# Kernel tuning notes

Measured on AMD Instinct MI355X. Metric: run time of the kernel, lower is better.

Reference implementation:

```python
import jax, jax.numpy as jnp
import numpy as np

N_HEADS = 16

def setup_inputs() -> dict:
    key = jax.random.key(0)
    ks = jax.random.split(key, 5)
    C = 1024
    B, T = 2, 2048
    s_in = 1.0 / np.sqrt(C)
    x = jax.random.normal(ks[0], (B, T, C), dtype=jnp.float32)
    W_qkv = jax.random.normal(ks[1], (C, 3 * C), dtype=jnp.float32) * s_in
    b_qkv = jnp.zeros((3 * C,), dtype=jnp.float32)
    W_proj = jax.random.normal(ks[2], (C, C), dtype=jnp.float32) * s_in
    b_proj = jnp.zeros((C,), dtype=jnp.float32)
    return {"x": x, "W_qkv": W_qkv, "b_qkv": b_qkv, "W_proj": W_proj, "b_proj": b_proj}

def reference(x, W_qkv, b_qkv, W_proj, b_proj):
    B, T, C = x.shape
    H = N_HEADS
    D = C // H  # head dim
    qkv = x @ W_qkv + b_qkv                      # [B,T,3C]
    q, k, v = jnp.split(qkv, 3, axis=-1)
    # [B,T,C] -> [B,H,T,D]
    q = q.reshape(B, T, H, D).transpose(0, 2, 1, 3)
    k = k.reshape(B, T, H, D).transpose(0, 2, 1, 3)
    v = v.reshape(B, T, H, D).transpose(0, 2, 1, 3)
    scale = 1.0 / np.sqrt(D)
    att = jnp.einsum('bhqd,bhkd->bhqk', q, k) * scale  # [B,H,T,T]
    causal = jnp.tril(jnp.ones((T, T), dtype=bool))
    att = jnp.where(causal[None, None], att, -jnp.inf)
    att = jax.nn.softmax(att, axis=-1)
    y = jnp.einsum('bhqk,bhkd->bhqd', att, v)    # [B,H,T,D]
    y = y.transpose(0, 2, 1, 3).reshape(B, T, C)
    return y @ W_proj + b_proj
```

## Files before the change

kernel.cpp:

```cpp
#include <hip/hip_runtime.h>
#include <hip/hip_bf16.h>
#include <stdint.h>

#define DEVI __device__ __forceinline__

typedef __attribute__((ext_vector_type(8))) short bf16x8;
typedef __attribute__((ext_vector_type(4))) float f32x4;
typedef __attribute__((ext_vector_type(4))) short short4v;
typedef __attribute__((ext_vector_type(4))) float float4v;
typedef __attribute__((ext_vector_type(2))) unsigned int uint2v;

#define QSCALE 0.1803368801111204f

DEVI unsigned short f2bf(float f) {
  union { float f; unsigned u; } v; v.f = f;
  unsigned r = v.u + 0x7FFFu + ((v.u >> 16) & 1u);
  return (unsigned short)(r >> 16);
}

DEVI unsigned cvt_pk_bf16(float lo, float hi) {
  unsigned r;
  asm("v_cvt_pk_bf16_f32 %0, %1, %2" : "=v"(r) : "v"(lo), "v"(hi));
  return r;
}

DEVI void async16(unsigned short* lds, const unsigned short* g) {
  __builtin_amdgcn_global_load_lds(
      (const __attribute__((address_space(1))) void*)g,
      (__attribute__((address_space(3))) void*)lds, 16, 0, 0);
}

DEVI int xcd_swz_flat() {
  int orig = (int)blockIdx.x + (int)gridDim.x * (int)blockIdx.y;
  int cpx = ((int)gridDim.x * (int)gridDim.y) >> 3;
  return (orig & 7) * cpx + (orig >> 3);
}

__global__ void k_f32_to_bf16(const float* __restrict__ in,
                              unsigned short* __restrict__ out, int n4) {
  int i = blockIdx.x * 256 + threadIdx.x;
  if (i < n4) {
    float4v f = *reinterpret_cast<const float4v*>(in + (size_t)i * 4);
    short4v o;
#pragma unroll
    for (int j = 0; j < 4; ++j) o[j] = (short)f2bf(f[j]);
    *reinterpret_cast<short4v*>(out + (size_t)i * 4) = o;
  }
}

__global__ void k_wt2(const float* __restrict__ Wq, const float* __restrict__ Wp,
                      unsigned short* __restrict__ WqT, unsigned short* __restrict__ WpT) {
  __shared__ float tile[32][33];
  const int bx = (int)blockIdx.x;
  const float* W;
  unsigned short* Wt;
  int N, n0;
  if (bx < 96) { W = Wq; Wt = WqT; N = 3072; n0 = bx * 32; }
  else         { W = Wp; Wt = WpT; N = 1024; n0 = (bx - 96) * 32; }
  const int K = 1024, k0 = (int)blockIdx.y * 32;
  int r = threadIdx.x >> 5, c = threadIdx.x & 31;
#pragma unroll
  for (int i = 0; i < 4; ++i)
    tile[r + i * 8][c] = W[(size_t)(k0 + r + i * 8) * N + n0 + c];
  __syncthreads();
#pragma unroll
  for (int i = 0; i < 4; ++i)
    Wt[(size_t)(n0 + r + i * 8) * K + k0 + c] = f2bf(tile[c][r + i * 8]);
}

DEVI void stage_ab(unsigned short* AsB, unsigned short* BsB,
                   const unsigned short* Ab, const unsigned short* Bb,
                   int K, int k0, int tid) {
#pragma unroll
  for (int it = 0; it < 2; ++it) {
    int c = it * 256 + tid;
    int row = c >> 2, cc = (c & 3) * 8;
    async16(&AsB[c * 8], Ab + (size_t)row * K + k0 + cc);
    async16(&BsB[c * 8], Bb + (size_t)row * K + k0 + cc);
  }
}

__global__ void k_gemm(const unsigned short* __restrict__ A,
                       const unsigned short* __restrict__ Bt,
                       const float* __restrict__ bias,
                       unsigned short* __restrict__ qkv,
                       unsigned short* __restrict__ vt,
                       int M, int N, int K) {
  __shared__ __align__(16) unsigned short As[2][128 * 32];
  __shared__ __align__(16) unsigned short Bs[2][128 * 32];
  const int tid = threadIdx.x;
  const int swzf = xcd_swz_flat();
  const int m0 = (swzf / (int)gridDim.x) * 128, n0 = (swzf % (int)gridDim.x) * 128;
  const int lane = tid & 63, w = tid >> 6;
  const int wr = (w >> 1) * 64, wc = (w & 1) * 64;
  const int lr = lane & 15, lg = lane >> 4;
  f32x4 acc[4][4] = {};
  const unsigned short* Ab = A + (size_t)m0 * K;
  const unsigned short* Bb = Bt + (size_t)n0 * K;

  const int ns = K >> 5;
  stage_ab(As[0], Bs[0], Ab, Bb, K, 0, tid);
  stage_ab(As[1], Bs[1], Ab, Bb, K, 32, tid);
  asm volatile("s_waitcnt vmcnt(4)" ::: "memory");
  __builtin_amdgcn_s_barrier();
  __builtin_amdgcn_sched_barrier(0);

  for (int s = 0; s < ns; ++s) {
    const int cur = s & 1;
    bf16x8 af[4], bfr[4];
#pragma unroll
    for (int m = 0; m < 4; ++m)
      af[m] = *reinterpret_cast<const bf16x8*>(&As[cur][(wr + m * 16 + lr) * 32 + lg * 8]);
#pragma unroll
    for (int n = 0; n < 4; ++n)
      bfr[n] = *reinterpret_cast<const bf16x8*>(&Bs[cur][(wc + n * 16 + lr) * 32 + lg * 8]);
#pragma unroll
    for (int m = 0; m < 4; ++m)
#pragma unroll
      for (int n = 0; n < 4; ++n)
        acc[m][n] = __builtin_amdgcn_mfma_f32_16x16x32_bf16(af[m], bfr[n], acc[m][n], 0, 0, 0);
    __builtin_amdgcn_s_barrier();
    const int ks = (s + 2 < ns) ? (s + 2) * 32 : 0;
    stage_ab(As[cur], Bs[cur], Ab, Bb, K, ks, tid);
    asm volatile("s_waitcnt vmcnt(4)" ::: "memory");
    __builtin_amdgcn_s_barrier();
    __builtin_amdgcn_sched_barrier(0);
  }
#pragma unroll
  for (int n = 0; n < 4; ++n) {
    int col = n0 + wc + n * 16 + lr;
    float bv = bias[col];
    int sel = col >> 10, cc = col & 1023;
    int h = cc >> 6, d = cc & 63;
    if (sel < 2) {
      float sc = (sel == 0) ? QSCALE : 1.0f;
#pragma unroll
      for (int m = 0; m < 4; ++m) {
#pragma unroll
        for (int r = 0; r < 4; ++r) {
          int row = m0 + wr + m * 16 + lg * 4 + r;
          int bh = ((row >> 11) << 4) + h;
          int t = row & 2047;
          qkv[((size_t)(sel * 32 + bh) * 2048 + t) * 64 + d] = f2bf((acc[m][n][r] + bv) * sc);
        }
      }
    } else {
#pragma unroll
      for (int m = 0; m < 4; ++m) {
        int row0 = m0 + wr + m * 16 + lg * 4;
        int bh = ((row0 >> 11) << 4) + h;
        int t0 = row0 & 2047;
        short4v pk;
#pragma unroll
        for (int r = 0; r < 4; ++r) pk[r] = (short)f2bf(acc[m][n][r] + bv);
        *reinterpret_cast<short4v*>(&vt[((size_t)(bh * 64 + d)) * 2048 + t0]) = pk;
      }
    }
  }
}

__global__ __launch_bounds__(256)
void k_gemmP(const unsigned short* __restrict__ A,
             const unsigned short* __restrict__ Bt,
             const float* __restrict__ bias,
             float* __restrict__ O, int M, int N, int K) {
  __shared__ __align__(16) unsigned short As[2][128 * 32];
  __shared__ __align__(16) unsigned short Bs[2][64 * 32];
  const int tid = threadIdx.x;
  const int swzf = xcd_swz_flat();
  const int m0 = (swzf / (int)gridDim.x) * 128, n0 = (swzf % (int)gridDim.x) * 64;
  const int lane = tid & 63, w = tid >> 6;
  const int wr = (w >> 1) * 64, wc = (w & 1) * 32;
  const int lr = lane & 15, lg = lane >> 4;
  f32x4 acc[4][2] = {};
  const unsigned short* Ab = A + (size_t)m0 * K;
  const unsigned short* Bb = Bt + (size_t)n0 * K;

  auto stage = [&](unsigned short* AsB, unsigned short* BsB, int k0) {
#pragma unroll
    for (int it = 0; it < 2; ++it) {
      int c = it * 256 + tid;
      int row = c >> 2, cc = (c & 3) * 8;
      async16(&AsB[c * 8], Ab + (size_t)row * K + k0 + cc);
    }
    int row = tid >> 2, cc = (tid & 3) * 8;
    async16(&BsB[tid * 8], Bb + (size_t)row * K + k0 + cc);
  };

  const int ns = K >> 5;
  stage(As[0], Bs[0], 0);
  stage(As[1], Bs[1], 32);
  asm volatile("s_waitcnt vmcnt(3)" ::: "memory");
  __builtin_amdgcn_s_barrier();
  __builtin_amdgcn_sched_barrier(0);

  for (int s = 0; s < ns; ++s) {
    const int cur = s & 1;
    bf16x8 af[4], bfr[2];
#pragma unroll
    for (int m = 0; m < 4; ++m)
      af[m] = *reinterpret_cast<const bf16x8*>(&As[cur][(wr + m * 16 + lr) * 32 + lg * 8]);
#pragma unroll
    for (int n = 0; n < 2; ++n)
      bfr[n] = *reinterpret_cast<const bf16x8*>(&Bs[cur][(wc + n * 16 + lr) * 32 + lg * 8]);
#pragma unroll
    for (int m = 0; m < 4; ++m)
#pragma unroll
      for (int n = 0; n < 2; ++n)
        acc[m][n] = __builtin_amdgcn_mfma_f32_16x16x32_bf16(af[m], bfr[n], acc[m][n], 0, 0, 0);
    __builtin_amdgcn_s_barrier();
    const int ks = (s + 2 < ns) ? (s + 2) * 32 : 0;
    stage(As[cur], Bs[cur], ks);
    asm volatile("s_waitcnt vmcnt(3)" ::: "memory");
    __builtin_amdgcn_s_barrier();
    __builtin_amdgcn_sched_barrier(0);
  }
#pragma unroll
  for (int n = 0; n < 2; ++n) {
    int col = n0 + wc + n * 16 + lr;
    float bv = bias[col];
#pragma unroll
    for (int m = 0; m < 4; ++m)
#pragma unroll
      for (int r = 0; r < 4; ++r) {
        int row = m0 + wr + m * 16 + lg * 4 + r;
        O[(size_t)row * N + col] = acc[m][n][r] + bv;
      }
  }
}

DEVI void stage_kv(unsigned short* KsB, unsigned short* VsB,
                   const unsigned short* Kbh, const unsigned short* Vbh,
                   int k0, int tid, int srow, int gcol) {
  async16(&KsB[tid * 8], Kbh + (size_t)(k0 + srow) * 64 + gcol);
  async16(&VsB[tid * 8], Vbh + (size_t)srow * 2048 + k0 + gcol);
}

DEVI void attn_store(unsigned short* __restrict__ Y, int bh, int qw, int lg, int lr,
                     const f32x4* o, float l_run) {
  const int b = bh >> 4, h = bh & 15;
  float rl = 1.0f / l_run;
  float rlo[4];
#pragma unroll
  for (int r = 0; r < 4; ++r) rlo[r] = __shfl(rl, lg * 4 + r, 64);
#pragma unroll
  for (int r = 0; r < 4; ++r) {
    int t = qw + lg * 4 + r;
#pragma unroll
    for (int n = 0; n < 4; ++n)
      Y[((size_t)(b * 2048 + t)) * 1024 + h * 64 + n * 16 + lr] = f2bf(o[n][r] * rlo[r]);
  }
}

__global__ __launch_bounds__(512)
void k_attn(const unsigned short* __restrict__ Qg,
            const unsigned short* __restrict__ Kg,
            const unsigned short* __restrict__ Vtg,
            unsigned short* __restrict__ Y) {
  __shared__ __align__(16) unsigned short Ks[2][64 * 64];
  __shared__ __align__(16) unsigned short Vs[2][64 * 64];
  __shared__ __align__(16) unsigned short Ps[8][16 * 64];
  const int orig = (int)blockIdx.x;
  const int slot = orig >> 8;
  const int within = orig & 255;
  const int sw = (within & 7) * 32 + (within >> 3);
  const int bh = sw >> 3;
  const int xp = sw & 7;
  const int x = slot ? xp : (15 - xp);
  const int nkt = 2 * x + 2;
  const int tid = threadIdx.x, lane = tid & 63, w = tid >> 6;
  const int lr = lane & 15, lg = lane >> 4;
  const int swz = (lane & 7) * 8;
  const int psw = (lr & 7) * 8;
  const unsigned short* Kbh = Kg + (size_t)bh * 2048 * 64;
  const unsigned short* Vbh = Vtg + (size_t)bh * 64 * 2048;

  const int qw = x * 128 + w * 16;
  const unsigned short* Qrow = Qg + ((size_t)bh * 2048 + qw + lr) * 64;
  bf16x8 qa0 = *reinterpret_cast<const bf16x8*>(&Qrow[lg * 8]);
  bf16x8 qa1 = *reinterpret_cast<const bf16x8*>(&Qrow[32 + lg * 8]);

  float m_run = -1e30f, l_run = 0.f;
  f32x4 o[4] = {};

  const int srow = tid >> 3;
  const int gcol = ((tid & 7) ^ (srow & 7)) * 8;

  stage_kv(Ks[0], Vs[0], Kbh, Vbh, 0, tid, srow, gcol);
  stage_kv(Ks[1], Vs[1], Kbh, Vbh, 64, tid, srow, gcol);
  asm volatile("s_waitcnt vmcnt(2)" ::: "memory");
  __builtin_amdgcn_s_barrier();
  __builtin_amdgcn_sched_barrier(0);

  for (int t = 0; t < nkt; ++t) {
    const int cur = t & 1;
    const int k0 = t * 64;
    if (k0 <= qw + 15) {
      const unsigned short* KsC = Ks[cur];
      const unsigned short* VsC = Vs[cur];

      f32x4 s[4];
      __builtin_amdgcn_s_setprio(1);
#pragma unroll
      for (int n = 0; n < 4; ++n) {
        bf16x8 kb0 = *reinterpret_cast<const bf16x8*>(&KsC[(n * 16 + lr) * 64 + ((lg * 8) ^ swz)]);
        bf16x8 kb1 = *reinterpret_cast<const bf16x8*>(&KsC[(n * 16 + lr) * 64 + ((32 + lg * 8) ^ swz)]);
        f32x4 z = {0.f, 0.f, 0.f, 0.f};
        z = __builtin_amdgcn_mfma_f32_16x16x32_bf16(kb0, qa0, z, 0, 0, 0);
        z = __builtin_amdgcn_mfma_f32_16x16x32_bf16(kb1, qa1, z, 0, 0, 0);
        s[n] = z;
      }
      __builtin_amdgcn_s_setprio(0);
      if (k0 + 63 > qw) {
        const int klim = qw + lr - k0 - lg * 4;
#pragma unroll
        for (int n = 0; n < 4; ++n)
#pragma unroll
          for (int r = 0; r < 4; ++r)
            if (n * 16 + r > klim) s[n][r] = -1e30f;
      }
      float tmax = s[0][0];
#pragma unroll
      for (int n = 0; n < 4; ++n)
#pragma unroll
        for (int r = 0; r < 4; ++r) tmax = fmaxf(tmax, s[n][r]);
      tmax = fmaxf(tmax, __shfl_xor(tmax, 16, 64));
      tmax = fmaxf(tmax, __shfl_xor(tmax, 32, 64));
      if (__any(tmax > m_run + 11.5f)) {
        float mNew = fmaxf(m_run, tmax);
        float alpha = __builtin_exp2f(m_run - mNew);
        m_run = mNew;
        l_run *= alpha;
        float ao[4];
#pragma unroll
        for (int r = 0; r < 4; ++r) ao[r] = __shfl(alpha, lg * 4 + r, 64);
#pragma unroll
        for (int n = 0; n < 4; ++n)
#pragma unroll
          for (int r = 0; r < 4; ++r) o[n][r] *= ao[r];
      }
      float tsum = 0.f;
#pragma unroll
      for (int n = 0; n < 4; ++n)
#pragma unroll
        for (int r = 0; r < 4; ++r) {
          s[n][r] = __builtin_exp2f(s[n][r] - m_run);
          tsum += s[n][r];
        }
      tsum += __shfl_xor(tsum, 16, 64);
      tsum += __shfl_xor(tsum, 32, 64);
      l_run += tsum;
#pragma unroll
      for (int n = 0; n < 4; ++n) {
        uint2v pk;
        pk[0] = cvt_pk_bf16(s[n][0], s[n][1]);
        pk[1] = cvt_pk_bf16(s[n][2], s[n][3]);
        *reinterpret_cast<uint2v*>(&Ps[w][lr * 64 + ((n * 16 + lg * 4) ^ psw)]) = pk;
      }
      __builtin_amdgcn_s_setprio(1);
#pragma unroll
      for (int jj = 0; jj < 2; ++jj) {
        bf16x8 pa = *reinterpret_cast<const bf16x8*>(&Ps[w][lr * 64 + ((jj * 32 + lg * 8) ^ psw)]);
#pragma unroll
        for (int n = 0; n < 4; ++n) {
          bf16x8 vb = *reinterpret_cast<const bf16x8*>(
              &VsC[(n * 16 + lr) * 64 + ((jj * 32 + lg * 8) ^ swz)]);
          o[n] = __builtin_amdgcn_mfma_f32_16x16x32_bf16(pa, vb, o[n], 0, 0, 0);
        }
      }
      __builtin_amdgcn_s_setprio(0);
    }
    __builtin_amdgcn_s_barrier();
    {
      const int ts = (t + 2 < nkt) ? (t + 2) : 0;
      stage_kv(Ks[cur], Vs[cur], Kbh, Vbh, ts * 64, tid, srow, gcol);
    }
    asm volatile("s_waitcnt vmcnt(2)" ::: "memory");
    __builtin_amdgcn_s_barrier();
    __builtin_amdgcn_sched_barrier(0);
  }
  attn_store(Y, bh, qw, lg, lr, o, l_run);
}

extern "C" void kernel_launch(void* const* d_in, const int* in_sizes, int n_in,
                              void* d_out, int out_size, void* d_ws, size_t ws_size,
                              hipStream_t stream) {
  const float* x     = (const float*)d_in[0];
  const float* Wqkv  = (const float*)d_in[1];
  const float* bqkv  = (const float*)d_in[2];
  const float* Wproj = (const float*)d_in[3];
  const float* bproj = (const float*)d_in[4];
  float* out = (float*)d_out;

  uint8_t* ws = (uint8_t*)d_ws;
  unsigned short* xb     = (unsigned short*)(ws);
  unsigned short* wqkvT  = (unsigned short*)(ws + ((size_t)8  << 20));
  unsigned short* wprojT = (unsigned short*)(ws + ((size_t)14 << 20));
  unsigned short* qkvb   = (unsigned short*)(ws + ((size_t)16 << 20));
  unsigned short* vt     = (unsigned short*)(ws + ((size_t)32 << 20));

  k_f32_to_bf16<<<4096, 256, 0, stream>>>(x, xb, 1048576);
  k_wt2<<<dim3(128, 32), 256, 0, stream>>>(Wqkv, Wproj, wqkvT, wprojT);
  k_gemm<<<dim3(24, 32), 256, 0, stream>>>(xb, wqkvT, bqkv, qkvb, vt, 4096, 3072, 1024);
  k_attn<<<dim3(512, 1), 512, 0, stream>>>(qkvb, qkvb + (size_t)32 * 2048 * 64, vt, xb);
  k_gemmP<<<dim3(16, 32), 256, 0, stream>>>(xb, wprojT, bproj, out, 4096, 1024, 1024);
}
```

Before: 117.3 us.

## Split long causal query tiles across two blocks and merge partial softmax outputs

The attention grid is re-mapped so the eight longest causal query tiles of each head are split into two KV-range halves, giving 768 blocks instead of 512 balanced pairs. Each half writes an unnormalized bf16 partial output plus per-row max and sum. A new merge kernel then rescales and combines the two halves into Y. The aim is shorter per-block critical paths and better load balance across CUs. In exchange it adds an extra kernel launch, extra global traffic for the partials, and bf16 rounding of the unnormalized partial outputs.

New measurement: 127.7 us. 8.9% more time.

```diff
diff --git a/kernel.cpp b/kernel.cpp
--- a/kernel.cpp
+++ b/kernel.cpp
@@ -16,6 +16,10 @@
   union { float f; unsigned u; } v; v.f = f;
   unsigned r = v.u + 0x7FFFu + ((v.u >> 16) & 1u);
   return (unsigned short)(r >> 16);
+}
+
+DEVI float bf2f(unsigned short u) {
+  union { unsigned u; float f; } v; v.u = ((unsigned)u) << 16; return v.f;
 }
 
 DEVI unsigned cvt_pk_bf16(float lo, float hi) {
@@ -236,38 +240,25 @@
   async16(&VsB[tid * 8], Vbh + (size_t)srow * 2048 + k0 + gcol);
 }
 
-DEVI void attn_store(unsigned short* __restrict__ Y, int bh, int qw, int lg, int lr,
-                     const f32x4* o, float l_run) {
-  const int b = bh >> 4, h = bh & 15;
-  float rl = 1.0f / l_run;
-  float rlo[4];
-#pragma unroll
-  for (int r = 0; r < 4; ++r) rlo[r] = __shfl(rl, lg * 4 + r, 64);
-#pragma unroll
-  for (int r = 0; r < 4; ++r) {
-    int t = qw + lg * 4 + r;
-#pragma unroll
-    for (int n = 0; n < 4; ++n)
-      Y[((size_t)(b * 2048 + t)) * 1024 + h * 64 + n * 16 + lr] = f2bf(o[n][r] * rlo[r]);
-  }
-}
-
 __global__ __launch_bounds__(512)
 void k_attn(const unsigned short* __restrict__ Qg,
             const unsigned short* __restrict__ Kg,
             const unsigned short* __restrict__ Vtg,
-            unsigned short* __restrict__ Y) {
+            unsigned short* __restrict__ Y,
+            unsigned short* __restrict__ po,
+            float2* __restrict__ pml) {
   __shared__ __align__(16) unsigned short Ks[2][64 * 64];
   __shared__ __align__(16) unsigned short Vs[2][64 * 64];
   __shared__ __align__(16) unsigned short Ps[8][16 * 64];
   const int orig = (int)blockIdx.x;
-  const int slot = orig >> 8;
-  const int within = orig & 255;
-  const int sw = (within & 7) * 32 + (within >> 3);
-  const int bh = sw >> 3;
-  const int xp = sw & 7;
-  const int x = slot ? xp : (15 - xp);
-  const int nkt = 2 * x + 2;
+  const int sw = (orig & 7) * 96 + (orig >> 3);
+  const int bh = sw / 24;
+  const int j = sw - bh * 24;
+  int x, s, nsplit;
+  if (j < 16) { x = 15 - (j >> 1); s = j & 1; nsplit = 2; }
+  else        { x = 23 - j;        s = 0;     nsplit = 1; }
+  const int tA = (nsplit == 2 && s == 1) ? (x + 1) : 0;
+  const int tB = (nsplit == 2 && s == 0) ? (x + 1) : (2 * x + 2);
   const int tid = threadIdx.x, lane = tid & 63, w = tid >> 6;
   const int lr = lane & 15, lg = lane >> 4;
   const int swz = (lane & 7) * 8;
@@ -286,20 +277,20 @@
   const int srow = tid >> 3;
   const int gcol = ((tid & 7) ^ (srow & 7)) * 8;
 
-  stage_kv(Ks[0], Vs[0], Kbh, Vbh, 0, tid, srow, gcol);
-  stage_kv(Ks[1], Vs[1], Kbh, Vbh, 64, tid, srow, gcol);
+  stage_kv(Ks[0], Vs[0], Kbh, Vbh, tA * 64, tid, srow, gcol);
+  stage_kv(Ks[1], Vs[1], Kbh, Vbh, (tA + 1) * 64, tid, srow, gcol);
   asm volatile("s_waitcnt vmcnt(2)" ::: "memory");
   __builtin_amdgcn_s_barrier();
   __builtin_amdgcn_sched_barrier(0);
 
-  for (int t = 0; t < nkt; ++t) {
-    const int cur = t & 1;
+  for (int t = tA; t < tB; ++t) {
+    const int cur = (t - tA) & 1;
     const int k0 = t * 64;
     if (k0 <= qw + 15) {
       const unsigned short* KsC = Ks[cur];
       const unsigned short* VsC = Vs[cur];
 
-      f32x4 s[4];
+      f32x4 sc[4];
       __builtin_amdgcn_s_setprio(1);
 #pragma unroll
       for (int n = 0; n < 4; ++n) {
@@ -308,7 +299,7 @@
         f32x4 z = {0.f, 0.f, 0.f, 0.f};
         z = __builtin_amdgcn_mfma_f32_16x16x32_bf16(kb0, qa0, z, 0, 0, 0);
         z = __builtin_amdgcn_mfma_f32_16x16x32_bf16(kb1, qa1, z, 0, 0, 0);
-        s[n] = z;
+        sc[n] = z;
       }
       __builtin_amdgcn_s_setprio(0);
       if (k0 + 63 > qw) {
@@ -317,13 +308,13 @@
         for (int n = 0; n < 4; ++n)
 #pragma unroll
           for (int r = 0; r < 4; ++r)
-            if (n * 16 + r > klim) s[n][r] = -1e30f;
-      }
-      float tmax = s[0][0];
+            if (n * 16 + r > klim) sc[n][r] = -1e30f;
+      }
+      float tmax = sc[0][0];
 #pragma unroll
       for (int n = 0; n < 4; ++n)
 #pragma unroll
-        for (int r = 0; r < 4; ++r) tmax = fmaxf(tmax, s[n][r]);
+        for (int r = 0; r < 4; ++r) tmax = fmaxf(tmax, sc[n][r]);
       tmax = fmaxf(tmax, __shfl_xor(tmax, 16, 64));
       tmax = fmaxf(tmax, __shfl_xor(tmax, 32, 64));
       if (__any(tmax > m_run + 11.5f)) {
@@ -344,8 +335,8 @@
       for (int n = 0; n < 4; ++n)
 #pragma unroll
         for (int r = 0; r < 4; ++r) {
-          s[n][r] = __builtin_exp2f(s[n][r] - m_run);
-          tsum += s[n][r];
+          sc[n][r] = __builtin_exp2f(sc[n][r] - m_run);
+          tsum += sc[n][r];
         }
       tsum += __shfl_xor(tsum, 16, 64);
       tsum += __shfl_xor(tsum, 32, 64);
@@ -353,8 +344,8 @@
 #pragma unroll
       for (int n = 0; n < 4; ++n) {
         uint2v pk;
-        pk[0] = cvt_pk_bf16(s[n][0], s[n][1]);
-        pk[1] = cvt_pk_bf16(s[n][2], s[n][3]);
+        pk[0] = cvt_pk_bf16(sc[n][0], sc[n][1]);
+        pk[1] = cvt_pk_bf16(sc[n][2], sc[n][3]);
         *reinterpret_cast<uint2v*>(&Ps[w][lr * 64 + ((n * 16 + lg * 4) ^ psw)]) = pk;
       }
       __builtin_amdgcn_s_setprio(1);
@@ -372,14 +363,85 @@
     }
     __builtin_amdgcn_s_barrier();
     {
-      const int ts = (t + 2 < nkt) ? (t + 2) : 0;
+      const int ts = (t + 2 < tB) ? (t + 2) : tA;
       stage_kv(Ks[cur], Vs[cur], Kbh, Vbh, ts * 64, tid, srow, gcol);
     }
     asm volatile("s_waitcnt vmcnt(2)" ::: "memory");
     __builtin_amdgcn_s_barrier();
     __builtin_amdgcn_sched_barrier(0);
   }
-  attn_store(Y, bh, qw, lg, lr, o, l_run);
+  const int b = bh >> 4, h = bh & 15;
+  if (nsplit == 1) {
+    float rl = 1.0f / l_run;
+    float rlo[4];
+#pragma unroll
+    for (int r = 0; r < 4; ++r) rlo[r] = __shfl(rl, lg * 4 + r, 64);
+#pragma unroll
+    for (int r = 0; r < 4; ++r) {
+      int t = qw + lg * 4 + r;
+#pragma unroll
+      for (int n = 0; n < 4; ++n)
+        Y[((size_t)(b * 2048 + t)) * 1024 + h * 64 + n * 16 + lr] = f2bf(o[n][r] * rlo[r]);
+    }
+  } else {
+    const int g = bh * 8 + (x - 8);
+    if (lg == 0) {
+      float2 v; v.x = m_run; v.y = l_run;
+      pml[(g * 2 + s) * 128 + w * 16 + lr] = v;
+    }
+    float oo[4][4];
+#pragma unroll
+    for (int r = 0; r < 4; ++r)
+#pragma unroll
+      for (int n = 0; n < 4; ++n) oo[r][n] = o[n][r];
+    if (s == 0) {
+#pragma unroll
+      for (int r = 0; r < 4; ++r) {
+        int t = qw + lg * 4 + r;
+#pragma unroll
+        for (int n = 0; n < 4; ++n)
+          Y[((size_t)(b * 2048 + t)) * 1024 + h * 64 + n * 16 + lr] = f2bf(oo[r][n]);
+      }
+    } else {
+#pragma unroll
+      for (int r = 0; r < 4; ++r) {
+        int row = w * 16 + lg * 4 + r;
+#pragma unroll
+        for (int n = 0; n < 4; ++n)
+          po[((size_t)g * 128 + row) * 64 + n * 16 + lr] = f2bf(oo[r][n]);
+      }
+    }
+  }
+}
+
+__global__ __launch_bounds__(256)
+void k_merge(unsigned short* __restrict__ Y,
+             const unsigned short* __restrict__ po,
+             const float2* __restrict__ pml) {
+  const int g = (int)blockIdx.x;
+  const int bh = g >> 3, x = (g & 7) + 8;
+  const int b = bh >> 4, h = bh & 15;
+  const int row = threadIdx.x >> 1;
+  const int d0 = ((int)threadIdx.x & 1) * 32;
+  float2 p0 = pml[(g * 2 + 0) * 128 + row];
+  float2 p1 = pml[(g * 2 + 1) * 128 + row];
+  float m = fmaxf(p0.x, p1.x);
+  float a0 = __builtin_exp2f(p0.x - m), a1 = __builtin_exp2f(p1.x - m);
+  float inv = 1.0f / (p0.y * a0 + p1.y * a1);
+  float c0 = a0 * inv, c1 = a1 * inv;
+  size_t yb = ((size_t)(b * 2048 + x * 128 + row)) * 1024 + h * 64 + d0;
+  size_t pb = ((size_t)g * 128 + row) * 64 + d0;
+#pragma unroll
+  for (int i = 0; i < 4; ++i) {
+    bf16x8 yv = *reinterpret_cast<const bf16x8*>(&Y[yb + i * 8]);
+    bf16x8 pv = *reinterpret_cast<const bf16x8*>(&po[pb + i * 8]);
+    bf16x8 ov;
+#pragma unroll
+    for (int jj = 0; jj < 8; ++jj)
+      ov[jj] = (short)f2bf(bf2f((unsigned short)yv[jj]) * c0 +
+                           bf2f((unsigned short)pv[jj]) * c1);
+    *reinterpret_cast<bf16x8*>(&Y[yb + i * 8]) = ov;
+  }
 }
 
 extern "C" void kernel_launch(void* const* d_in, const int* in_sizes, int n_in,
@@ -398,10 +460,13 @@
   unsigned short* wprojT = (unsigned short*)(ws + ((size_t)14 << 20));
   unsigned short* qkvb   = (unsigned short*)(ws + ((size_t)16 << 20));
   unsigned short* vt     = (unsigned short*)(ws + ((size_t)32 << 20));
+  unsigned short* po     = (unsigned short*)(ws + ((size_t)8  << 20));
+  float2*         pml    = (float2*)(ws + ((size_t)12 << 20));
 
   k_f32_to_bf16<<<4096, 256, 0, stream>>>(x, xb, 1048576);
   k_wt2<<<dim3(128, 32), 256, 0, stream>>>(Wqkv, Wproj, wqkvT, wprojT);
   k_gemm<<<dim3(24, 32), 256, 0, stream>>>(xb, wqkvT, bqkv, qkvb, vt, 4096, 3072, 1024);
-  k_attn<<<dim3(512, 1), 512, 0, stream>>>(qkvb, qkvb + (size_t)32 * 2048 * 64, vt, xb);
+  k_attn<<<dim3(768, 1), 512, 0, stream>>>(qkvb, qkvb + (size_t)32 * 2048 * 64, vt, xb, po, pml);
+  k_merge<<<dim3(256, 1), 256, 0, stream>>>(xb, po, pml);
   k_gemmP<<<dim3(16, 32), 256, 0, stream>>>(xb, wprojT, bproj, out, 4096, 1024, 1024);
 }
```
